# Optimization experiments

Hardware: AMD Instinct MI355X
Metric: run time of the kernel (lower is better)

Reference implementation:

```python
import jax, jax.numpy as jnp
import numpy as np

# ---- static config (mirrors Net.__init__) ----
N_NODES, N_EDGES = 4000, 20000
N_PROTS, D = 919, 512            # node_emb: Embedding(919, 512); F_in = D (divide_input=False)
TOWERS, F_OUT = 4, D // 4        # F_out = out_channels // towers = 128
EDGE_D = 50
N_GRAPHS, N_CLASSES = 32, 10
N_LAYERS = 2
EPS_BN, EPS_STD = 1e-5, 1e-5

# deg histogram passed to PNAConv; only avg_deg['log'] matters for the scalers used
DEG_HIST = np.array([0., 800., 1200., 900., 600., 300., 150., 50.])
AVG_DEG_LOG = float((np.log(np.arange(DEG_HIST.size) + 1.0) * DEG_HIST).sum() / DEG_HIST.sum())


def setup_inputs() -> dict:
    key = jax.random.key(0)
    ks = jax.random.split(key, 16)
    g = lambda i, shape, s=0.05: (jax.random.normal(ks[i], shape, jnp.float32) * s)
    return dict(
        node_emb_w=g(0, (N_PROTS, D), 0.1),
        edge_emb_w=g(1, (2, EDGE_D), 0.1),
        pe_w=g(2, (2, D)), pe_b=jnp.zeros((D,), jnp.float32),
        edge_enc_w=g(3, (N_LAYERS, EDGE_D, D)), edge_enc_b=jnp.zeros((N_LAYERS, D), jnp.float32),
        pre_w=g(4, (N_LAYERS, TOWERS, 3 * D, D)), pre_b=jnp.zeros((N_LAYERS, TOWERS, D), jnp.float32),
        post_w=g(5, (N_LAYERS, TOWERS, 13 * D, F_OUT)), post_b=jnp.zeros((N_LAYERS, TOWERS, F_OUT), jnp.float32),
        lin_w=g(6, (N_LAYERS, D, D)), lin_b=jnp.zeros((N_LAYERS, D), jnp.float32),
        bn_gamma=jnp.ones((N_LAYERS, D), jnp.float32), bn_beta=jnp.zeros((N_LAYERS, D), jnp.float32),
        acts=jax.random.normal(ks[7], (N_NODES, 2), jnp.float32),
        fc1_w=g(8, (D, 2 * D)), fc1_b=jnp.zeros((2 * D,), jnp.float32),
        fc_out_w=g(9, (2 * D, N_CLASSES)), fc_out_b=jnp.zeros((N_CLASSES,), jnp.float32),
        prelu_a=jnp.float32(0.25),
        global_idx=jax.random.randint(ks[10], (N_NODES,), 0, N_PROTS),
        sign=jax.random.randint(ks[11], (N_EDGES,), 0, 2),
        edge_index=jax.random.randint(ks[12], (2, N_EDGES), 0, N_NODES),
        batch=jnp.sort(jax.random.randint(ks[13], (N_NODES,), 0, N_GRAPHS)),
    )


def _pna_layer(x, src, dst, e, pre_w, pre_b, post_w, post_b, lin_w, lin_b):
    # x: [N, D], e: [E, D] (edge_encoder output), pre_w: [T, 3D, D], post_w: [T, 13D, F_OUT]
    N, E = x.shape[0], src.shape[0]
    # pre-NN on cat([x_i, x_j, edge_attr]) expressed as split matmuls (pre_layers=1 -> single Linear)
    Wi, Wj, We = pre_w[:, :D], pre_w[:, D:2 * D], pre_w[:, 2 * D:]
    m = (jnp.einsum('ef,tfd->etd', x[dst], Wi)
         + jnp.einsum('ef,tfd->etd', x[src], Wj)
         + jnp.einsum('ef,tfd->etd', e, We) + pre_b)          # [E, T, D]
    # multi-aggregation at destination nodes: mean / min / max / std
    cnt = jax.ops.segment_sum(jnp.ones((E,), m.dtype), dst, N)  # in-degree
    has = (cnt > 0)[:, None, None]
    deg = jnp.maximum(cnt, 1.0)[:, None, None]                  # clamp(1) as in PyG
    s1 = jax.ops.segment_sum(m, dst, N)
    s2 = jax.ops.segment_sum(m * m, dst, N)
    mean = s1 / deg
    std = jnp.sqrt(jax.nn.relu(s2 / deg - mean * mean) + EPS_STD)
    mn = jnp.where(has, jax.ops.segment_min(m, dst, N), 0.0)
    mx = jnp.where(has, jax.ops.segment_max(m, dst, N), 0.0)
    agg = jnp.concatenate([mean, mn, mx, std], axis=-1)         # [N, T, 4D]
    # degree scalers: identity, amplification, attenuation
    amp = jnp.log(deg + 1.0) / AVG_DEG_LOG
    out = jnp.concatenate([agg, agg * amp, agg / amp], axis=-1)  # [N, T, 12D]
    # post-NN on cat([x, out]) as split matmuls (post_layers=1)
    Wx, Wo = post_w[:, :D], post_w[:, D:]
    o = (jnp.einsum('nf,tfd->ntd', x, Wx)
         + jnp.einsum('ntf,tfd->ntd', out, Wo) + post_b)        # [N, T, F_OUT]
    return o.reshape(N, TOWERS * F_OUT) @ lin_w + lin_b         # [N, D]


def reference(node_emb_w, edge_emb_w, pe_w, pe_b, edge_enc_w, edge_enc_b,
              pre_w, pre_b, post_w, post_b, lin_w, lin_b, bn_gamma, bn_beta,
              acts, fc1_w, fc1_b, fc_out_w, fc_out_b, prelu_a,
              global_idx, sign, edge_index, batch):
    src, dst = edge_index[0], edge_index[1]
    x = node_emb_w[global_idx] + (acts @ pe_w + pe_b)           # node_emb + PostEncoding
    ea = edge_emb_w[sign]                                       # [E, 50]
    for l in range(N_LAYERS):
        e = ea @ edge_enc_w[l] + edge_enc_b[l]                  # shared edge encoder
        h = _pna_layer(x, src, dst, e, pre_w[l], pre_b[l], post_w[l], post_b[l], lin_w[l], lin_b[l])
        mu = h.mean(axis=0)
        var = ((h - mu) ** 2).mean(axis=0)                      # training-mode BatchNorm (biased var)
        x = jax.nn.relu(bn_gamma[l] * (h - mu) * jax.lax.rsqrt(var + EPS_BN) + bn_beta[l])
    pooled = jax.ops.segment_sum(x, batch, N_GRAPHS)            # global_add_pool
    z = pooled @ fc1_w + fc1_b
    z = jnp.where(z > 0, z, prelu_a * z)                        # PReLU
    logits = z @ fc_out_w + fc_out_b
    return jax.nn.log_softmax(logits, axis=-1)
```

## Files before the change

### kernel.cpp

```cpp
#include <hip/hip_runtime.h>
#include <hip/hip_bf16.h>
#include <float.h>

#define NN 4000
#define NE 20000
#define DD 512
#define NT 4
#define FO 128
#define NG 32
#define NC 10
#define XGW 4608
#define AVGLOG 1.2548916493836102f
#define EPS_STD_ 1e-5f
#define EPS_BN_ 1e-5f

typedef __bf16 bf16x8 __attribute__((ext_vector_type(8)));
typedef float  f32x4  __attribute__((ext_vector_type(4)));

__device__ __forceinline__ void async_copy16(const void* g, void* l) {
    __builtin_amdgcn_global_load_lds((const __attribute__((address_space(1))) void*)g,
                                     (__attribute__((address_space(3))) void*)l, 16, 0, 0);
}

template<int OUT_BF16, int HAS_BIAS>
__device__ __forceinline__ void mfma_core(
    const __bf16* __restrict__ A, int lda,
    const __bf16* __restrict__ BT, int ldbt,
    void* __restrict__ Cv, int ldc,
    const float* __restrict__ bias,
    int M, int K, int m0, int n0)
{
    __shared__ __bf16 As[128 * 32];
    __shared__ __bf16 Bs[128 * 32];
    const int tid = threadIdx.x;
    const int wave = tid >> 6, lane = tid & 63;
    const int wm = (wave >> 1) * 64, wn = (wave & 1) * 64;
    const int fr = lane & 15, fq = lane >> 4;
    const int fk = fq * 8;
    const int srow = lane >> 2;
    const int skc = (lane & 3) * 8;

    f32x4 acc[4][4];
    const f32x4 zero = {0.f, 0.f, 0.f, 0.f};
#pragma unroll
    for (int i = 0; i < 4; ++i)
#pragma unroll
        for (int j = 0; j < 4; ++j) acc[i][j] = zero;

    for (int k0 = 0; k0 < K; k0 += 32) {
#pragma unroll
        for (int q = 0; q < 2; ++q) {
            const int row = wave * 32 + q * 16 + srow;
            int ar = m0 + row; if (ar > M - 1) ar = M - 1;
            async_copy16(A + (size_t)ar * lda + k0 + skc, As + wave * 1024 + q * 512);
            async_copy16(BT + (size_t)(n0 + row) * ldbt + k0 + skc, Bs + wave * 1024 + q * 512);
        }
        __syncthreads();
        bf16x8 af[4], bfr[4];
#pragma unroll
        for (int mi = 0; mi < 4; ++mi) af[mi]  = *(const bf16x8*)(As + (wm + mi * 16 + fr) * 32 + fk);
#pragma unroll
        for (int ni = 0; ni < 4; ++ni) bfr[ni] = *(const bf16x8*)(Bs + (wn + ni * 16 + fr) * 32 + fk);
#pragma unroll
        for (int mi = 0; mi < 4; ++mi)
#pragma unroll
            for (int ni = 0; ni < 4; ++ni)
                acc[mi][ni] = __builtin_amdgcn_mfma_f32_16x16x32_bf16(af[mi], bfr[ni], acc[mi][ni], 0, 0, 0);
        __syncthreads();
    }
    float* Cf = (float*)Cv; __bf16* Cb = (__bf16*)Cv;
#pragma unroll
    for (int mi = 0; mi < 4; ++mi) {
#pragma unroll
        for (int ni = 0; ni < 4; ++ni) {
            const int col = n0 + wn + ni * 16 + fr;
            const int rb = m0 + wm + mi * 16 + fq * 4;
            const float bv = HAS_BIAS ? bias[col] : 0.f;
#pragma unroll
            for (int r = 0; r < 4; ++r) {
                const int rowc = rb + r;
                if (rowc < M) {
                    const float v = acc[mi][ni][r] + bv;
                    if (OUT_BF16) Cb[(size_t)rowc * ldc + col] = (__bf16)v;
                    else          Cf[(size_t)rowc * ldc + col] = v;
                }
            }
        }
    }
}

__global__ __launch_bounds__(256) void k_xg(const __bf16* __restrict__ XB, const __bf16* __restrict__ WCAT,
                                            __bf16* __restrict__ XG) {
    mfma_core<1, 0>(XB, 512, WCAT, 512, XG, XGW, nullptr, NN, 512,
                    blockIdx.y * 128, blockIdx.x * 128);
}

__global__ __launch_bounds__(256) void k_gw(const __bf16* __restrict__ AB, const __bf16* __restrict__ WTT,
                                            float* __restrict__ GWP) {
    const int t = blockIdx.z & 3, kh = blockIdx.z >> 2;
    const __bf16* A  = AB  + (size_t)t * 2048 + (size_t)kh * 1024;
    const __bf16* BT = WTT + (size_t)t * 384 * 2048 + (size_t)kh * 1024;
    float* C = GWP + (size_t)blockIdx.z * NN * 384;
    mfma_core<0, 0>(A, 8192, BT, 2048, C, 384, nullptr, NN, 1024,
                    blockIdx.y * 128, blockIdx.x * 128);
}

__global__ __launch_bounds__(256) void k_lin(const __bf16* __restrict__ OB, const __bf16* __restrict__ WLINT,
                                             const float* __restrict__ bl, float* __restrict__ H) {
    mfma_core<0, 1>(OB, 512, WLINT, 512, H, 512, bl, NN, 512,
                    blockIdx.y * 128, blockIdx.x * 128);
}

__device__ __forceinline__ void tr32(const float* __restrict__ S, int sld,
                                     __bf16* __restrict__ D, int dld) {
    __shared__ float t[32][33];
    const int x = threadIdx.x, y0 = threadIdx.y * 4;
#pragma unroll
    for (int i = 0; i < 4; ++i) t[y0 + i][x] = S[(size_t)(y0 + i) * sld + x];
    __syncthreads();
#pragma unroll
    for (int i = 0; i < 4; ++i) D[(size_t)(y0 + i) * dld + x] = (__bf16)t[x][y0 + i];
}

__global__ void k_tr(const float* __restrict__ pw, const float* __restrict__ pow_,
                     const float* __restrict__ lw,
                     __bf16* __restrict__ WCAT, __bf16* __restrict__ WTT, __bf16* __restrict__ WLINT) {
    int id = blockIdx.x;
    if (id < 2048) {
        const int z = id >> 8, r = id & 255;
        const int t = z & 3, half = z >> 2;
        const int x = r & 15, y = r >> 4;
        const float* S = pw + ((size_t)(t * 1536 + half * 512 + y * 32)) * 512 + x * 32;
        __bf16* D = WCAT + ((size_t)(half * 2048 + t * 512 + x * 32)) * 512 + y * 32;
        tr32(S, 512, D, 512);
    } else if (id < 2304) {
        const int id3 = id - 2048;
        const int t = id3 >> 6, r = id3 & 63;
        const int x = r & 3, y = r >> 2;
        const float* S = pow_ + ((size_t)(t * 6656 + y * 32)) * 128 + x * 32;
        __bf16* D = WCAT + ((size_t)(4096 + t * 128 + x * 32)) * 512 + y * 32;
        tr32(S, 128, D, 512);
    } else if (id < 5376) {
        const int id4 = id - 2304;
        const int z = id4 >> 8, r = id4 & 255;
        const int t = z / 3, w = z % 3;
        const int x = r & 3, y = r >> 2;
        const float* S = pow_ + ((size_t)(t * 6656 + 512 + w * 2048 + y * 32)) * 128 + x * 32;
        __bf16* D = WTT + (size_t)t * 384 * 2048 + ((size_t)(w * 128 + x * 32)) * 2048 + y * 32;
        tr32(S, 128, D, 2048);
    } else {
        const int r = id - 5376;
        const int x = r & 15, y = r >> 4;
        const float* S = lw + (size_t)y * 32 * 512 + x * 32;
        __bf16* D = WLINT + (size_t)x * 32 * 512 + y * 32;
        tr32(S, 512, D, 512);
    }
}

__global__ void k_count(const int* __restrict__ dst, int* __restrict__ cnt) {
    int e = blockIdx.x * 256 + threadIdx.x;
    if (e < NE) atomicAdd(&cnt[dst[e]], 1);
}

__global__ __launch_bounds__(1024) void k_scan(const int* __restrict__ cnt, int* __restrict__ offs,
                                               float* __restrict__ amp, float* __restrict__ ramp) {
    __shared__ int part[1024];
    const int t = threadIdx.x;
    const int base = t * 4;
    int loc[4]; int s = 0;
#pragma unroll
    for (int i = 0; i < 4; ++i) { int v = (base + i < NN) ? cnt[base + i] : 0; loc[i] = s; s += v; }
    part[t] = s;
    __syncthreads();
    for (int o = 1; o < 1024; o <<= 1) {
        int v = (t >= o) ? part[t - o] : 0;
        __syncthreads();
        part[t] += v;
        __syncthreads();
    }
    const int pre = (t > 0) ? part[t - 1] : 0;
#pragma unroll
    for (int i = 0; i < 4; ++i) if (base + i < NN) offs[base + i] = pre + loc[i];
    if (t == 1023) offs[NN] = part[1023];
    for (int n = t; n < NN; n += 1024) {
        float deg = fmaxf((float)cnt[n], 1.0f);
        float a = logf(deg + 1.0f) / AVGLOG;
        amp[n] = a; ramp[n] = 1.0f / a;
    }
}

__global__ void k_fill(const int* __restrict__ src, const int* __restrict__ dst,
                       const int* __restrict__ sgn, const int* __restrict__ offs,
                       int* __restrict__ fill, int* __restrict__ esrc, int* __restrict__ esgn) {
    int e = blockIdx.x * 256 + threadIdx.x;
    if (e < NE) {
        int d = dst[e];
        int pos = offs[d] + atomicAdd(&fill[d], 1);
        esrc[pos] = src[e];
        esgn[pos] = sgn[e];
    }
}

__global__ void k_build_x(const float* __restrict__ nemb, const float* __restrict__ acts,
                          const float* __restrict__ pew, const float* __restrict__ peb,
                          const int* __restrict__ gidx, float* __restrict__ X, __bf16* __restrict__ XB) {
    int idx = blockIdx.x * 256 + threadIdx.x;
    int n = idx >> 9, d = idx & 511;
    float v = nemb[(size_t)gidx[n] * DD + d] + acts[n * 2] * pew[d] + acts[n * 2 + 1] * pew[DD + d] + peb[d];
    X[idx] = v; XB[idx] = (__bf16)v;
}

__global__ __launch_bounds__(256) void k_ekem(const float* __restrict__ eemb, const float* __restrict__ eew,
                                              const float* __restrict__ eeb, const float* __restrict__ pw,
                                              const float* __restrict__ pb, float* __restrict__ EM) {
    __shared__ float EKs[1024];
    const int tid = threadIdx.x;
    for (int i = tid; i < 1024; i += 256) {
        int k = i >> 9, d = i & 511;
        float s = eeb[d];
        for (int f = 0; f < 50; ++f) s += eemb[k * 50 + f] * eew[(size_t)f * 512 + d];
        EKs[i] = s;
    }
    __syncthreads();
    const int idx = blockIdx.x * 256 + tid;
    const int k = idx >> 11, g = idx & 2047;
    const int t = g >> 9, d = g & 511;
    const float* ek = EKs + k * 512;
    const float* W = pw + ((size_t)t * 1536 + 1024) * 512 + d;
    float s = pb[g];
    for (int f = 0; f < 512; ++f) s += ek[f] * W[(size_t)f * 512];
    EM[idx] = s;
}

__global__ __launch_bounds__(256) void k_agg(const __bf16* __restrict__ XG, const float* __restrict__ EM,
                                             const int* __restrict__ offs, const int* __restrict__ cnt,
                                             const int* __restrict__ esrc, const int* __restrict__ esgn,
                                             __bf16* __restrict__ AB) {
    const int n = blockIdx.x;
    const int g = threadIdx.x * 8;
    float xid[8], em0[8], em1[8];
    {
        bf16x8 xb = *(const bf16x8*)(XG + (size_t)n * XGW + g);
#pragma unroll
        for (int i = 0; i < 8; ++i) xid[i] = (float)xb[i];
    }
    *(float4*)&em0[0] = *(const float4*)&EM[g];
    *(float4*)&em0[4] = *(const float4*)&EM[g + 4];
    *(float4*)&em1[0] = *(const float4*)&EM[2048 + g];
    *(float4*)&em1[4] = *(const float4*)&EM[2048 + g + 4];
    float s1[8], s2[8], mn[8], mx[8];
#pragma unroll
    for (int i = 0; i < 8; ++i) { s1[i] = 0.f; s2[i] = 0.f; mn[i] = FLT_MAX; mx[i] = -FLT_MAX; }
    const int j0 = offs[n], j1 = offs[n + 1];
    for (int j = j0; j < j1; ++j) {
        const int s = esrc[j];
        const int sg = esgn[j];
        bf16x8 xv = *(const bf16x8*)(XG + (size_t)s * XGW + 2048 + g);
#pragma unroll
        for (int i = 0; i < 8; ++i) {
            float m = xid[i] + (float)xv[i] + (sg ? em1[i] : em0[i]);
            s1[i] += m; s2[i] += m * m;
            mn[i] = fminf(mn[i], m); mx[i] = fmaxf(mx[i], m);
        }
    }
    const int c = cnt[n];
    const float deg = fmaxf((float)c, 1.0f);
    const float rdeg = 1.0f / deg;
    bf16x8 vmean, vmn, vmx, vsd;
#pragma unroll
    for (int i = 0; i < 8; ++i) {
        float mean = s1[i] * rdeg;
        float var = s2[i] * rdeg - mean * mean;
        float sd = sqrtf(fmaxf(var, 0.f) + EPS_STD_);
        float mnv = (c == 0) ? 0.f : mn[i];
        float mxv = (c == 0) ? 0.f : mx[i];
        vmean[i] = (__bf16)mean; vmn[i] = (__bf16)mnv; vmx[i] = (__bf16)mxv; vsd[i] = (__bf16)sd;
    }
    const int t = g >> 9, d = g & 511;
    __bf16* base = AB + (size_t)n * 8192 + (size_t)t * 2048 + d;
    *(bf16x8*)(base + 0 * DD) = vmean;
    *(bf16x8*)(base + 1 * DD) = vmn;
    *(bf16x8*)(base + 2 * DD) = vmx;
    *(bf16x8*)(base + 3 * DD) = vsd;
}

__global__ void k_combine(const __bf16* __restrict__ XG, const float* __restrict__ GWP,
                          const float* __restrict__ amp, const float* __restrict__ ramp,
                          const float* __restrict__ pb, __bf16* __restrict__ OB) {
    int idx = blockIdx.x * 256 + threadIdx.x;
    int n = idx >> 9, c = idx & 511;
    int t = c >> 7, o = c & 127;
    const float* ga = GWP + ((size_t)t) * NN * 384 + (size_t)n * 384;
    const float* gb = GWP + ((size_t)(4 + t)) * NN * 384 + (size_t)n * 384;
    float w1 = ga[o] + gb[o];
    float w2 = ga[128 + o] + gb[128 + o];
    float w3 = ga[256 + o] + gb[256 + o];
    float gx = (float)XG[(size_t)n * XGW + 4096 + c];
    float v = gx + w1 + amp[n] * w2 + ramp[n] * w3 + pb[c];
    OB[idx] = (__bf16)v;
}

__global__ void k_bnstat(const float* __restrict__ H, float* __restrict__ BN) {
    int cidx = blockIdx.x * 256 + threadIdx.x;
    int r0 = blockIdx.y * 125;
    float s = 0.f, q = 0.f;
    for (int r = r0; r < r0 + 125; ++r) { float v = H[(size_t)r * DD + cidx]; s += v; q += v * v; }
    atomicAdd(&BN[cidx], s); atomicAdd(&BN[DD + cidx], q);
}

__global__ void k_bnapply(const float* __restrict__ H, const float* __restrict__ BN,
                          const float* __restrict__ gamma, const float* __restrict__ beta,
                          float* __restrict__ X, __bf16* __restrict__ XB) {
    int idx = blockIdx.x * 256 + threadIdx.x;
    int d = idx & 511;
    float mu = BN[d] * (1.0f / NN);
    float var = BN[DD + d] * (1.0f / NN) - mu * mu;
    float v = gamma[d] * (H[idx] - mu) * rsqrtf(var + EPS_BN_) + beta[d];
    v = fmaxf(v, 0.f);
    X[idx] = v; XB[idx] = (__bf16)v;
}

__global__ void k_pool(const float* __restrict__ X, const int* __restrict__ batch, float* __restrict__ PL) {
    int idx = blockIdx.x * 256 + threadIdx.x;
    int n = idx >> 9, d = idx & 511;
    atomicAdd(&PL[(size_t)batch[n] * DD + d], X[idx]);
}

__global__ void k_fc1(const float* __restrict__ PL, const float* __restrict__ W1,
                      const float* __restrict__ b1, const float* __restrict__ pa, float* __restrict__ Z) {
    int idx = blockIdx.x * 256 + threadIdx.x;
    int g = idx >> 10, j = idx & 1023;
    float s = b1[j];
    const float* p = PL + (size_t)g * DD;
    for (int f = 0; f < DD; ++f) s += p[f] * W1[(size_t)f * 1024 + j];
    float a = *pa;
    Z[idx] = s > 0.f ? s : a * s;
}

__global__ __launch_bounds__(64) void k_out(const float* __restrict__ Z, const float* __restrict__ Wo,
                                            const float* __restrict__ bo, float* __restrict__ out) {
    int g = blockIdx.x, t = threadIdx.x;
    float part[NC];
#pragma unroll
    for (int c = 0; c < NC; ++c) part[c] = 0.f;
    for (int f = t; f < 1024; f += 64) {
        float zv = Z[g * 1024 + f];
#pragma unroll
        for (int c = 0; c < NC; ++c) part[c] += zv * Wo[(size_t)f * NC + c];
    }
#pragma unroll
    for (int off = 32; off > 0; off >>= 1)
#pragma unroll
        for (int c = 0; c < NC; ++c) part[c] += __shfl_down(part[c], off);
    if (t == 0) {
        float lg[NC], mxv = -FLT_MAX;
#pragma unroll
        for (int c = 0; c < NC; ++c) { lg[c] = part[c] + bo[c]; mxv = fmaxf(mxv, lg[c]); }
        float se = 0.f;
#pragma unroll
        for (int c = 0; c < NC; ++c) se += expf(lg[c] - mxv);
        float lse = mxv + logf(se);
#pragma unroll
        for (int c = 0; c < NC; ++c) out[g * NC + c] = lg[c] - lse;
    }
}

extern "C" void kernel_launch(void* const* d_in, const int* in_sizes, int n_in,
                              void* d_out, int out_size, void* d_ws, size_t ws_size,
                              hipStream_t stream) {
    const float* node_emb_w = (const float*)d_in[0];
    const float* edge_emb_w = (const float*)d_in[1];
    const float* pe_w   = (const float*)d_in[2];
    const float* pe_b   = (const float*)d_in[3];
    const float* edge_enc_w = (const float*)d_in[4];
    const float* edge_enc_b = (const float*)d_in[5];
    const float* pre_w  = (const float*)d_in[6];
    const float* pre_b  = (const float*)d_in[7];
    const float* post_w = (const float*)d_in[8];
    const float* post_b = (const float*)d_in[9];
    const float* lin_w  = (const float*)d_in[10];
    const float* lin_b  = (const float*)d_in[11];
    const float* bn_gamma = (const float*)d_in[12];
    const float* bn_beta  = (const float*)d_in[13];
    const float* acts   = (const float*)d_in[14];
    const float* fc1_w  = (const float*)d_in[15];
    const float* fc1_b  = (const float*)d_in[16];
    const float* fc_out_w = (const float*)d_in[17];
    const float* fc_out_b = (const float*)d_in[18];
    const float* prelu_a  = (const float*)d_in[19];
    const int* global_idx = (const int*)d_in[20];
    const int* sgn        = (const int*)d_in[21];
    const int* edge_index = (const int*)d_in[22];
    const int* batch      = (const int*)d_in[23];
    float* out = (float*)d_out;

    char* W = (char*)d_ws;
    size_t off = 0;
    auto alloc = [&](size_t bytes) { void* p = W + off; off += (bytes + 63) & ~(size_t)63; return p; };
    float*  X     = (float*)alloc((size_t)NN * DD * 4);
    __bf16* XB    = (__bf16*)alloc((size_t)NN * DD * 2);
    float*  H     = (float*)alloc((size_t)NN * DD * 4);
    __bf16* XG    = (__bf16*)alloc((size_t)NN * XGW * 2);
    __bf16* AB    = (__bf16*)alloc((size_t)NN * 8192 * 2);
    float*  GWP   = (float*)alloc((size_t)8 * NN * 384 * 4);
    __bf16* OB    = (__bf16*)alloc((size_t)NN * DD * 2);
    __bf16* WCAT  = (__bf16*)alloc((size_t)XGW * 512 * 2);
    __bf16* WTT   = (__bf16*)alloc((size_t)NT * 384 * 2048 * 2);
    __bf16* WLINT = (__bf16*)alloc((size_t)512 * 512 * 2);
    float*  EM    = (float*)alloc(2 * 2048 * 4);
    float*  BN    = (float*)alloc(2 * 512 * 4);
    float*  PL    = (float*)alloc((size_t)NG * DD * 4);
    float*  ZB    = (float*)alloc((size_t)NG * 1024 * 4);
    float*  AMP   = (float*)alloc(NN * 4);
    float*  RAMP  = (float*)alloc(NN * 4);
    int*    CNT   = (int*)alloc(NN * 4);
    int*    OFFS  = (int*)alloc((NN + 1) * 4);
    int*    FILL  = (int*)alloc(NN * 4);
    int*    ESRC  = (int*)alloc(NE * 4);
    int*    ESGN  = (int*)alloc(NE * 4);

    const int* src = edge_index;
    const int* dst = edge_index + NE;

    hipMemsetAsync(CNT, 0, NN * sizeof(int), stream);
    hipMemsetAsync(FILL, 0, NN * sizeof(int), stream);
    k_count<<<(NE + 255) / 256, 256, 0, stream>>>(dst, CNT);
    k_scan<<<1, 1024, 0, stream>>>(CNT, OFFS, AMP, RAMP);
    k_fill<<<(NE + 255) / 256, 256, 0, stream>>>(src, dst, sgn, OFFS, FILL, ESRC, ESGN);
    k_build_x<<<NN * DD / 256, 256, 0, stream>>>(node_emb_w, acts, pe_w, pe_b, global_idx, X, XB);

    for (int l = 0; l < 2; ++l) {
        const float* pre_w_l  = pre_w  + (size_t)l * NT * 3 * DD * DD;
        const float* pre_b_l  = pre_b  + (size_t)l * NT * DD;
        const float* post_w_l = post_w + (size_t)l * NT * 6656 * FO;
        const float* post_b_l = post_b + (size_t)l * NT * FO;
        const float* lin_w_l  = lin_w  + (size_t)l * DD * DD;
        const float* lin_b_l  = lin_b  + (size_t)l * DD;
        const float* eew_l    = edge_enc_w + (size_t)l * 50 * DD;
        const float* eeb_l    = edge_enc_b + (size_t)l * DD;

        k_tr<<<5632, dim3(32, 8), 0, stream>>>(pre_w_l, post_w_l, lin_w_l, WCAT, WTT, WLINT);
        k_ekem<<<16, 256, 0, stream>>>(edge_emb_w, eew_l, eeb_l, pre_w_l, pre_b_l, EM);

        k_xg<<<dim3(36, 32), 256, 0, stream>>>(XB, WCAT, XG);
        k_agg<<<NN, 256, 0, stream>>>(XG, EM, OFFS, CNT, ESRC, ESGN, AB);
        k_gw<<<dim3(3, 32, 8), 256, 0, stream>>>(AB, WTT, GWP);
        k_combine<<<NN * DD / 256, 256, 0, stream>>>(XG, GWP, AMP, RAMP, post_b_l, OB);
        k_lin<<<dim3(4, 32), 256, 0, stream>>>(OB, WLINT, lin_b_l, H);

        hipMemsetAsync(BN, 0, 2 * DD * sizeof(float), stream);
        k_bnstat<<<dim3(2, 32), 256, 0, stream>>>(H, BN);
        k_bnapply<<<NN * DD / 256, 256, 0, stream>>>(H, BN, bn_gamma + (size_t)l * DD, bn_beta + (size_t)l * DD, X, XB);
    }

    hipMemsetAsync(PL, 0, NG * DD * sizeof(float), stream);
    k_pool<<<NN * DD / 256, 256, 0, stream>>>(X, batch, PL);
    k_fc1<<<NG * 1024 / 256, 256, 0, stream>>>(PL, fc1_w, fc1_b, prelu_a, ZB);
    k_out<<<NG, 64, 0, stream>>>(ZB, fc_out_w, fc_out_b, out);
}
```

Before: 570.5 us.

## Fuse combine, BN stats, pooling and head into GEMM epilogues and merge launches

The tower GEMM k_gw is rewritten as a full-K 32x384 tile that applies the scaler combine in its epilogue, which removes the split-K fp32 partial buffer and the separate combine kernel. k_lin now accumulates batch-norm sums in its epilogue, k_bnapply pools directly on the last layer, and fc1, the output layer and log_softmax are merged into one head kernel. The build_x work is merged into the scan launch, the fp32 X buffer is dropped, and the edge-matrix kernel is parallelised across 64 blocks. The cost is fewer blocks in k_gw (500, each running a long K loop), which may reduce occupancy and latency hiding.

Result: slower. 582.2 us (+2.0%).

```diff
diff --git a/kernel.cpp b/kernel.cpp
--- a/kernel.cpp
+++ b/kernel.cpp
@@ -22,12 +22,10 @@
                                      (__attribute__((address_space(3))) void*)l, 16, 0, 0);
 }
 
-template<int OUT_BF16, int HAS_BIAS>
-__device__ __forceinline__ void mfma_core(
+__device__ __forceinline__ void mfma_core128(
     const __bf16* __restrict__ A, int lda,
     const __bf16* __restrict__ BT, int ldbt,
-    void* __restrict__ Cv, int ldc,
-    const float* __restrict__ bias,
+    __bf16* __restrict__ C, int ldc,
     int M, int K, int m0, int n0)
 {
     __shared__ __bf16 As[128 * 32];
@@ -68,47 +66,176 @@
                 acc[mi][ni] = __builtin_amdgcn_mfma_f32_16x16x32_bf16(af[mi], bfr[ni], acc[mi][ni], 0, 0, 0);
         __syncthreads();
     }
-    float* Cf = (float*)Cv; __bf16* Cb = (__bf16*)Cv;
 #pragma unroll
     for (int mi = 0; mi < 4; ++mi) {
 #pragma unroll
         for (int ni = 0; ni < 4; ++ni) {
             const int col = n0 + wn + ni * 16 + fr;
             const int rb = m0 + wm + mi * 16 + fq * 4;
-            const float bv = HAS_BIAS ? bias[col] : 0.f;
 #pragma unroll
             for (int r = 0; r < 4; ++r) {
                 const int rowc = rb + r;
-                if (rowc < M) {
+                if (rowc < M) C[(size_t)rowc * ldc + col] = (__bf16)acc[mi][ni][r];
+            }
+        }
+    }
+}
+
+__global__ __launch_bounds__(256) void k_xg(const __bf16* __restrict__ XB, const __bf16* __restrict__ WCAT,
+                                            __bf16* __restrict__ XG) {
+    mfma_core128(XB, 512, WCAT, 512, XG, XGW, NN, 512, blockIdx.y * 128, blockIdx.x * 128);
+}
+
+__global__ __launch_bounds__(256) void k_gw(const __bf16* __restrict__ AB, const __bf16* __restrict__ WTT,
+                                            const __bf16* __restrict__ XG,
+                                            const float* __restrict__ amp, const float* __restrict__ ramp,
+                                            const float* __restrict__ pb, __bf16* __restrict__ OB,
+                                            float* __restrict__ BN, float* __restrict__ PL, int zero_pl) {
+    const int t = blockIdx.y;
+    const int n0 = blockIdx.x * 32;
+    __shared__ __bf16 As[32 * 32];
+    __shared__ __bf16 Bs[384 * 32];
+    __shared__ float  Ep[32][388];
+    const int tid = threadIdx.x;
+    const int wave = tid >> 6, lane = tid & 63;
+    const int fr = lane & 15, fq = lane >> 4;
+    const int wn = wave * 96;
+
+    f32x4 acc[2][6];
+    const f32x4 zero = {0.f, 0.f, 0.f, 0.f};
+#pragma unroll
+    for (int i = 0; i < 2; ++i)
+#pragma unroll
+        for (int j = 0; j < 6; ++j) acc[i][j] = zero;
+
+    const __bf16* Abase = AB + (size_t)n0 * 8192 + (size_t)t * 2048;
+    const __bf16* Bbase = WTT + (size_t)t * 384 * 2048;
+    const int ar = tid >> 2, akc = (tid & 3) * 8;
+
+    for (int k0 = 0; k0 < 2048; k0 += 32) {
+        if (wave < 2)
+            async_copy16(Abase + (size_t)ar * 8192 + k0 + akc, As + tid * 8);
+#pragma unroll
+        for (int i = 0; i < 6; ++i) {
+            const int cb = tid + 256 * i;
+            const int br = cb >> 2, bkc = (cb & 3) * 8;
+            async_copy16(Bbase + (size_t)br * 2048 + k0 + bkc, Bs + cb * 8);
+        }
+        __syncthreads();
+        bf16x8 a[2], b[6];
+#pragma unroll
+        for (int mi = 0; mi < 2; ++mi) a[mi] = *(const bf16x8*)(As + (mi * 16 + fr) * 32 + fq * 8);
+#pragma unroll
+        for (int ni = 0; ni < 6; ++ni) b[ni] = *(const bf16x8*)(Bs + (wn + ni * 16 + fr) * 32 + fq * 8);
+#pragma unroll
+        for (int mi = 0; mi < 2; ++mi)
+#pragma unroll
+            for (int ni = 0; ni < 6; ++ni)
+                acc[mi][ni] = __builtin_amdgcn_mfma_f32_16x16x32_bf16(a[mi], b[ni], acc[mi][ni], 0, 0, 0);
+        __syncthreads();
+    }
+#pragma unroll
+    for (int mi = 0; mi < 2; ++mi)
+#pragma unroll
+        for (int ni = 0; ni < 6; ++ni)
+#pragma unroll
+            for (int r = 0; r < 4; ++r)
+                Ep[mi * 16 + fq * 4 + r][wn + ni * 16 + fr] = acc[mi][ni][r];
+    __syncthreads();
+    const int row = tid >> 3, o0 = (tid & 7) * 16;
+    const int n = n0 + row;
+    const float av = amp[n], rv = ramp[n];
+    bf16x8 gx0 = *(const bf16x8*)(XG + (size_t)n * XGW + 4096 + t * 128 + o0);
+    bf16x8 gx1 = *(const bf16x8*)(XG + (size_t)n * XGW + 4096 + t * 128 + o0 + 8);
+    bf16x8 ov0, ov1;
+#pragma unroll
+    for (int u = 0; u < 8; ++u) {
+        int o = o0 + u;
+        float v = (float)gx0[u] + Ep[row][o] + av * Ep[row][128 + o] + rv * Ep[row][256 + o] + pb[t * 128 + o];
+        ov0[u] = (__bf16)v;
+    }
+#pragma unroll
+    for (int u = 0; u < 8; ++u) {
+        int o = o0 + 8 + u;
+        float v = (float)gx1[u] + Ep[row][o] + av * Ep[row][128 + o] + rv * Ep[row][256 + o] + pb[t * 128 + o];
+        ov1[u] = (__bf16)v;
+    }
+    *(bf16x8*)(OB + (size_t)n * 512 + t * 128 + o0) = ov0;
+    *(bf16x8*)(OB + (size_t)n * 512 + t * 128 + o0 + 8) = ov1;
+    if (blockIdx.x == 0 && blockIdx.y == 0) {
+        BN[tid] = 0.f; BN[256 + tid] = 0.f; BN[512 + tid] = 0.f; BN[768 + tid] = 0.f;
+        if (zero_pl)
+            for (int i = tid; i < NG * DD; i += 256) PL[i] = 0.f;
+    }
+}
+
+__global__ __launch_bounds__(256) void k_lin(const __bf16* __restrict__ OB, const __bf16* __restrict__ WLINT,
+                                             const float* __restrict__ bl, float* __restrict__ H,
+                                             float* __restrict__ BN) {
+    const int n0c = blockIdx.x * 128, m0 = blockIdx.y * 64;
+    __shared__ __bf16 As[64 * 32];
+    __shared__ __bf16 Bs[128 * 32];
+    __shared__ float bnS[128], bnQ[128];
+    const int tid = threadIdx.x;
+    if (tid < 128) { bnS[tid] = 0.f; bnQ[tid] = 0.f; }
+    const int wave = tid >> 6, lane = tid & 63;
+    const int wr = wave >> 1, wc = wave & 1;
+    const int fr = lane & 15, fq = lane >> 4;
+    f32x4 acc[2][4];
+    const f32x4 zero = {0.f, 0.f, 0.f, 0.f};
+#pragma unroll
+    for (int i = 0; i < 2; ++i)
+#pragma unroll
+        for (int j = 0; j < 4; ++j) acc[i][j] = zero;
+
+    const int ar = tid >> 2, akc = (tid & 3) * 8;
+    int arow = m0 + ar; if (arow > NN - 1) arow = NN - 1;
+    for (int k0 = 0; k0 < 512; k0 += 32) {
+        async_copy16(OB + (size_t)arow * 512 + k0 + akc, As + tid * 8);
+#pragma unroll
+        for (int i = 0; i < 2; ++i) {
+            const int cb = tid + 256 * i;
+            const int br = cb >> 2, bkc = (cb & 3) * 8;
+            async_copy16(WLINT + (size_t)(n0c + br) * 512 + k0 + bkc, Bs + cb * 8);
+        }
+        __syncthreads();
+        bf16x8 a[2], b[4];
+#pragma unroll
+        for (int mi = 0; mi < 2; ++mi) a[mi] = *(const bf16x8*)(As + (wr * 32 + mi * 16 + fr) * 32 + fq * 8);
+#pragma unroll
+        for (int ni = 0; ni < 4; ++ni) b[ni] = *(const bf16x8*)(Bs + (wc * 64 + ni * 16 + fr) * 32 + fq * 8);
+#pragma unroll
+        for (int mi = 0; mi < 2; ++mi)
+#pragma unroll
+            for (int ni = 0; ni < 4; ++ni)
+                acc[mi][ni] = __builtin_amdgcn_mfma_f32_16x16x32_bf16(a[mi], b[ni], acc[mi][ni], 0, 0, 0);
+        __syncthreads();
+    }
+#pragma unroll
+    for (int ni = 0; ni < 4; ++ni) {
+        const int lc = wc * 64 + ni * 16 + fr;
+        const int col = n0c + lc;
+        const float bv = bl[col];
+        float s = 0.f, q = 0.f;
+#pragma unroll
+        for (int mi = 0; mi < 2; ++mi) {
+#pragma unroll
+            for (int r = 0; r < 4; ++r) {
+                const int rowc = m0 + wr * 32 + mi * 16 + fq * 4 + r;
+                if (rowc < NN) {
                     const float v = acc[mi][ni][r] + bv;
-                    if (OUT_BF16) Cb[(size_t)rowc * ldc + col] = (__bf16)v;
-                    else          Cf[(size_t)rowc * ldc + col] = v;
+                    H[(size_t)rowc * 512 + col] = v;
+                    s += v; q += v * v;
                 }
             }
         }
-    }
-}
-
-__global__ __launch_bounds__(256) void k_xg(const __bf16* __restrict__ XB, const __bf16* __restrict__ WCAT,
-                                            __bf16* __restrict__ XG) {
-    mfma_core<1, 0>(XB, 512, WCAT, 512, XG, XGW, nullptr, NN, 512,
-                    blockIdx.y * 128, blockIdx.x * 128);
-}
-
-__global__ __launch_bounds__(256) void k_gw(const __bf16* __restrict__ AB, const __bf16* __restrict__ WTT,
-                                            float* __restrict__ GWP) {
-    const int t = blockIdx.z & 3, kh = blockIdx.z >> 2;
-    const __bf16* A  = AB  + (size_t)t * 2048 + (size_t)kh * 1024;
-    const __bf16* BT = WTT + (size_t)t * 384 * 2048 + (size_t)kh * 1024;
-    float* C = GWP + (size_t)blockIdx.z * NN * 384;
-    mfma_core<0, 0>(A, 8192, BT, 2048, C, 384, nullptr, NN, 1024,
-                    blockIdx.y * 128, blockIdx.x * 128);
-}
-
-__global__ __launch_bounds__(256) void k_lin(const __bf16* __restrict__ OB, const __bf16* __restrict__ WLINT,
-                                             const float* __restrict__ bl, float* __restrict__ H) {
-    mfma_core<0, 1>(OB, 512, WLINT, 512, H, 512, bl, NN, 512,
-                    blockIdx.y * 128, blockIdx.x * 128);
+        atomicAdd(&bnS[lc], s); atomicAdd(&bnQ[lc], q);
+    }
+    __syncthreads();
+    if (tid < 128) {
+        atomicAdd(&BN[n0c + tid], bnS[tid]);
+        atomicAdd(&BN[512 + n0c + tid], bnQ[tid]);
+    }
 }
 
 __device__ __forceinline__ void tr32(const float* __restrict__ S, int sld,
@@ -162,30 +289,40 @@
     if (e < NE) atomicAdd(&cnt[dst[e]], 1);
 }
 
-__global__ __launch_bounds__(1024) void k_scan(const int* __restrict__ cnt, int* __restrict__ offs,
-                                               float* __restrict__ amp, float* __restrict__ ramp) {
-    __shared__ int part[1024];
+__global__ __launch_bounds__(1024) void k_scan_bx(const int* __restrict__ cnt, int* __restrict__ offs,
+                                                  float* __restrict__ amp, float* __restrict__ ramp,
+                                                  const float* __restrict__ nemb, const float* __restrict__ acts,
+                                                  const float* __restrict__ pew, const float* __restrict__ peb,
+                                                  const int* __restrict__ gidx, __bf16* __restrict__ XB) {
     const int t = threadIdx.x;
-    const int base = t * 4;
-    int loc[4]; int s = 0;
-#pragma unroll
-    for (int i = 0; i < 4; ++i) { int v = (base + i < NN) ? cnt[base + i] : 0; loc[i] = s; s += v; }
-    part[t] = s;
-    __syncthreads();
-    for (int o = 1; o < 1024; o <<= 1) {
-        int v = (t >= o) ? part[t - o] : 0;
-        __syncthreads();
-        part[t] += v;
-        __syncthreads();
-    }
-    const int pre = (t > 0) ? part[t - 1] : 0;
-#pragma unroll
-    for (int i = 0; i < 4; ++i) if (base + i < NN) offs[base + i] = pre + loc[i];
-    if (t == 1023) offs[NN] = part[1023];
-    for (int n = t; n < NN; n += 1024) {
-        float deg = fmaxf((float)cnt[n], 1.0f);
-        float a = logf(deg + 1.0f) / AVGLOG;
-        amp[n] = a; ramp[n] = 1.0f / a;
+    if (blockIdx.x == 0) {
+        __shared__ int part[1024];
+        const int base = t * 4;
+        int loc[4]; int s = 0;
+#pragma unroll
+        for (int i = 0; i < 4; ++i) { int v = (base + i < NN) ? cnt[base + i] : 0; loc[i] = s; s += v; }
+        part[t] = s;
+        __syncthreads();
+        for (int o = 1; o < 1024; o <<= 1) {
+            int v = (t >= o) ? part[t - o] : 0;
+            __syncthreads();
+            part[t] += v;
+            __syncthreads();
+        }
+        const int pre = (t > 0) ? part[t - 1] : 0;
+#pragma unroll
+        for (int i = 0; i < 4; ++i) if (base + i < NN) offs[base + i] = pre + loc[i];
+        if (t == 1023) offs[NN] = part[1023];
+        for (int n = t; n < NN; n += 1024) {
+            float deg = fmaxf((float)cnt[n], 1.0f);
+            float a = logf(deg + 1.0f) / AVGLOG;
+            amp[n] = a; ramp[n] = 1.0f / a;
+        }
+    } else {
+        const int idx = (blockIdx.x - 1) * 1024 + t;
+        const int n = idx >> 9, d = idx & 511;
+        float v = nemb[(size_t)gidx[n] * DD + d] + acts[n * 2] * pew[d] + acts[n * 2 + 1] * pew[DD + d] + peb[d];
+        XB[idx] = (__bf16)v;
     }
 }
 
@@ -201,35 +338,36 @@
     }
 }
 
-__global__ void k_build_x(const float* __restrict__ nemb, const float* __restrict__ acts,
-                          const float* __restrict__ pew, const float* __restrict__ peb,
-                          const int* __restrict__ gidx, float* __restrict__ X, __bf16* __restrict__ XB) {
-    int idx = blockIdx.x * 256 + threadIdx.x;
-    int n = idx >> 9, d = idx & 511;
-    float v = nemb[(size_t)gidx[n] * DD + d] + acts[n * 2] * pew[d] + acts[n * 2 + 1] * pew[DD + d] + peb[d];
-    X[idx] = v; XB[idx] = (__bf16)v;
-}
-
-__global__ __launch_bounds__(256) void k_ekem(const float* __restrict__ eemb, const float* __restrict__ eew,
-                                              const float* __restrict__ eeb, const float* __restrict__ pw,
-                                              const float* __restrict__ pb, float* __restrict__ EM) {
-    __shared__ float EKs[1024];
+__global__ __launch_bounds__(256) void k_em(const float* __restrict__ eemb, const float* __restrict__ eew,
+                                            const float* __restrict__ eeb, const float* __restrict__ pw,
+                                            const float* __restrict__ pb, float* __restrict__ EM) {
+    __shared__ float eks[512];
+    __shared__ float part[4][64];
     const int tid = threadIdx.x;
-    for (int i = tid; i < 1024; i += 256) {
-        int k = i >> 9, d = i & 511;
-        float s = eeb[d];
-        for (int f = 0; f < 50; ++f) s += eemb[k * 50 + f] * eew[(size_t)f * 512 + d];
-        EKs[i] = s;
-    }
-    __syncthreads();
-    const int idx = blockIdx.x * 256 + tid;
-    const int k = idx >> 11, g = idx & 2047;
+    const int k = blockIdx.x >> 5;
+    const int g0 = (blockIdx.x & 31) * 64;
+#pragma unroll
+    for (int h = 0; h < 2; ++h) {
+        const int f = tid + h * 256;
+        float s = eeb[f];
+        for (int c = 0; c < 50; ++c) s += eemb[k * 50 + c] * eew[(size_t)c * 512 + f];
+        eks[f] = s;
+    }
+    __syncthreads();
+    const int wave = tid >> 6, lane = tid & 63;
+    const int g = g0 + lane;
     const int t = g >> 9, d = g & 511;
-    const float* ek = EKs + k * 512;
-    const float* W = pw + ((size_t)t * 1536 + 1024) * 512 + d;
-    float s = pb[g];
-    for (int f = 0; f < 512; ++f) s += ek[f] * W[(size_t)f * 512];
-    EM[idx] = s;
+    const float* Wp = pw + ((size_t)(t * 1536 + 1024)) * 512 + d;
+    float s = 0.f;
+    const int f0 = wave * 128;
+#pragma unroll 4
+    for (int f = f0; f < f0 + 128; ++f) s += eks[f] * Wp[(size_t)f * 512];
+    part[wave][lane] = s;
+    __syncthreads();
+    if (tid < 64) {
+        const int gg = g0 + tid;
+        EM[k * 2048 + gg] = pb[gg] + part[0][tid] + part[1][tid] + part[2][tid] + part[3][tid];
+    }
 }
 
 __global__ __launch_bounds__(256) void k_agg(const __bf16* __restrict__ XG, const float* __restrict__ EM,
@@ -284,84 +422,73 @@
     *(bf16x8*)(base + 3 * DD) = vsd;
 }
 
-__global__ void k_combine(const __bf16* __restrict__ XG, const float* __restrict__ GWP,
-                          const float* __restrict__ amp, const float* __restrict__ ramp,
-                          const float* __restrict__ pb, __bf16* __restrict__ OB) {
-    int idx = blockIdx.x * 256 + threadIdx.x;
-    int n = idx >> 9, c = idx & 511;
-    int t = c >> 7, o = c & 127;
-    const float* ga = GWP + ((size_t)t) * NN * 384 + (size_t)n * 384;
-    const float* gb = GWP + ((size_t)(4 + t)) * NN * 384 + (size_t)n * 384;
-    float w1 = ga[o] + gb[o];
-    float w2 = ga[128 + o] + gb[128 + o];
-    float w3 = ga[256 + o] + gb[256 + o];
-    float gx = (float)XG[(size_t)n * XGW + 4096 + c];
-    float v = gx + w1 + amp[n] * w2 + ramp[n] * w3 + pb[c];
-    OB[idx] = (__bf16)v;
-}
-
-__global__ void k_bnstat(const float* __restrict__ H, float* __restrict__ BN) {
-    int cidx = blockIdx.x * 256 + threadIdx.x;
-    int r0 = blockIdx.y * 125;
-    float s = 0.f, q = 0.f;
-    for (int r = r0; r < r0 + 125; ++r) { float v = H[(size_t)r * DD + cidx]; s += v; q += v * v; }
-    atomicAdd(&BN[cidx], s); atomicAdd(&BN[DD + cidx], q);
-}
-
 __global__ void k_bnapply(const float* __restrict__ H, const float* __restrict__ BN,
                           const float* __restrict__ gamma, const float* __restrict__ beta,
-                          float* __restrict__ X, __bf16* __restrict__ XB) {
+                          __bf16* __restrict__ XB, float* __restrict__ PL,
+                          const int* __restrict__ batch, int last) {
     int idx = blockIdx.x * 256 + threadIdx.x;
-    int d = idx & 511;
+    int n = idx >> 9, d = idx & 511;
     float mu = BN[d] * (1.0f / NN);
-    float var = BN[DD + d] * (1.0f / NN) - mu * mu;
+    float var = BN[512 + d] * (1.0f / NN) - mu * mu;
     float v = gamma[d] * (H[idx] - mu) * rsqrtf(var + EPS_BN_) + beta[d];
     v = fmaxf(v, 0.f);
-    X[idx] = v; XB[idx] = (__bf16)v;
-}
-
-__global__ void k_pool(const float* __restrict__ X, const int* __restrict__ batch, float* __restrict__ PL) {
-    int idx = blockIdx.x * 256 + threadIdx.x;
-    int n = idx >> 9, d = idx & 511;
-    atomicAdd(&PL[(size_t)batch[n] * DD + d], X[idx]);
-}
-
-__global__ void k_fc1(const float* __restrict__ PL, const float* __restrict__ W1,
-                      const float* __restrict__ b1, const float* __restrict__ pa, float* __restrict__ Z) {
-    int idx = blockIdx.x * 256 + threadIdx.x;
-    int g = idx >> 10, j = idx & 1023;
-    float s = b1[j];
-    const float* p = PL + (size_t)g * DD;
-    for (int f = 0; f < DD; ++f) s += p[f] * W1[(size_t)f * 1024 + j];
-    float a = *pa;
-    Z[idx] = s > 0.f ? s : a * s;
-}
-
-__global__ __launch_bounds__(64) void k_out(const float* __restrict__ Z, const float* __restrict__ Wo,
-                                            const float* __restrict__ bo, float* __restrict__ out) {
-    int g = blockIdx.x, t = threadIdx.x;
-    float part[NC];
-#pragma unroll
-    for (int c = 0; c < NC; ++c) part[c] = 0.f;
-    for (int f = t; f < 1024; f += 64) {
-        float zv = Z[g * 1024 + f];
-#pragma unroll
-        for (int c = 0; c < NC; ++c) part[c] += zv * Wo[(size_t)f * NC + c];
+    if (last) atomicAdd(&PL[(size_t)batch[n] * DD + d], v);
+    else XB[idx] = (__bf16)v;
+}
+
+__global__ __launch_bounds__(256) void k_head(const float* __restrict__ PL, const float* __restrict__ W1,
+                                              const float* __restrict__ b1, const float* __restrict__ Wo,
+                                              const float* __restrict__ bo, const float* __restrict__ pa,
+                                              float* __restrict__ out) {
+    __shared__ float pl[512];
+    __shared__ float zz[1024];
+    __shared__ float lgs[NC];
+    const int g = blockIdx.x, tid = threadIdx.x;
+    pl[tid] = PL[(size_t)g * 512 + tid];
+    pl[tid + 256] = PL[(size_t)g * 512 + 256 + tid];
+    if (tid < NC) lgs[tid] = bo[tid];
+    __syncthreads();
+    const float a = *pa;
+#pragma unroll
+    for (int h = 0; h < 4; ++h) {
+        const int j = tid + h * 256;
+        float s0 = 0.f, s1 = 0.f, s2 = 0.f, s3 = 0.f;
+        for (int f = 0; f < 512; f += 4) {
+            s0 += pl[f + 0] * W1[(size_t)(f + 0) * 1024 + j];
+            s1 += pl[f + 1] * W1[(size_t)(f + 1) * 1024 + j];
+            s2 += pl[f + 2] * W1[(size_t)(f + 2) * 1024 + j];
+            s3 += pl[f + 3] * W1[(size_t)(f + 3) * 1024 + j];
+        }
+        float s = b1[j] + ((s0 + s1) + (s2 + s3));
+        zz[j] = s > 0.f ? s : a * s;
+    }
+    __syncthreads();
+    float p[NC];
+#pragma unroll
+    for (int c = 0; c < NC; ++c) p[c] = 0.f;
+    for (int f = tid; f < 1024; f += 256) {
+        const float z = zz[f];
+#pragma unroll
+        for (int c = 0; c < NC; ++c) p[c] += z * Wo[(size_t)f * NC + c];
     }
 #pragma unroll
     for (int off = 32; off > 0; off >>= 1)
 #pragma unroll
-        for (int c = 0; c < NC; ++c) part[c] += __shfl_down(part[c], off);
-    if (t == 0) {
-        float lg[NC], mxv = -FLT_MAX;
-#pragma unroll
-        for (int c = 0; c < NC; ++c) { lg[c] = part[c] + bo[c]; mxv = fmaxf(mxv, lg[c]); }
+        for (int c = 0; c < NC; ++c) p[c] += __shfl_down(p[c], off);
+    if ((tid & 63) == 0)
+#pragma unroll
+        for (int c = 0; c < NC; ++c) atomicAdd(&lgs[c], p[c]);
+    __syncthreads();
+    if (tid == 0) {
+        float mxv = -FLT_MAX;
+#pragma unroll
+        for (int c = 0; c < NC; ++c) mxv = fmaxf(mxv, lgs[c]);
         float se = 0.f;
 #pragma unroll
-        for (int c = 0; c < NC; ++c) se += expf(lg[c] - mxv);
-        float lse = mxv + logf(se);
-#pragma unroll
-        for (int c = 0; c < NC; ++c) out[g * NC + c] = lg[c] - lse;
+        for (int c = 0; c < NC; ++c) se += expf(lgs[c] - mxv);
+        const float lse = mxv + logf(se);
+#pragma unroll
+        for (int c = 0; c < NC; ++c) out[g * NC + c] = lgs[c] - lse;
     }
 }
 
@@ -397,37 +524,33 @@
     char* W = (char*)d_ws;
     size_t off = 0;
     auto alloc = [&](size_t bytes) { void* p = W + off; off += (bytes + 63) & ~(size_t)63; return p; };
-    float*  X     = (float*)alloc((size_t)NN * DD * 4);
     __bf16* XB    = (__bf16*)alloc((size_t)NN * DD * 2);
     float*  H     = (float*)alloc((size_t)NN * DD * 4);
     __bf16* XG    = (__bf16*)alloc((size_t)NN * XGW * 2);
     __bf16* AB    = (__bf16*)alloc((size_t)NN * 8192 * 2);
-    float*  GWP   = (float*)alloc((size_t)8 * NN * 384 * 4);
     __bf16* OB    = (__bf16*)alloc((size_t)NN * DD * 2);
     __bf16* WCAT  = (__bf16*)alloc((size_t)XGW * 512 * 2);
     __bf16* WTT   = (__bf16*)alloc((size_t)NT * 384 * 2048 * 2);
     __bf16* WLINT = (__bf16*)alloc((size_t)512 * 512 * 2);
     float*  EM    = (float*)alloc(2 * 2048 * 4);
-    float*  BN    = (float*)alloc(2 * 512 * 4);
+    float*  BN    = (float*)alloc(1024 * 4);
     float*  PL    = (float*)alloc((size_t)NG * DD * 4);
-    float*  ZB    = (float*)alloc((size_t)NG * 1024 * 4);
     float*  AMP   = (float*)alloc(NN * 4);
     float*  RAMP  = (float*)alloc(NN * 4);
     int*    CNT   = (int*)alloc(NN * 4);
+    int*    FILL  = (int*)alloc(NN * 4);
     int*    OFFS  = (int*)alloc((NN + 1) * 4);
-    int*    FILL  = (int*)alloc(NN * 4);
     int*    ESRC  = (int*)alloc(NE * 4);
     int*    ESGN  = (int*)alloc(NE * 4);
 
     const int* src = edge_index;
     const int* dst = edge_index + NE;
 
-    hipMemsetAsync(CNT, 0, NN * sizeof(int), stream);
-    hipMemsetAsync(FILL, 0, NN * sizeof(int), stream);
+    hipMemsetAsync(CNT, 0, 2 * NN * sizeof(int), stream);
     k_count<<<(NE + 255) / 256, 256, 0, stream>>>(dst, CNT);
-    k_scan<<<1, 1024, 0, stream>>>(CNT, OFFS, AMP, RAMP);
+    k_scan_bx<<<2001, 1024, 0, stream>>>(CNT, OFFS, AMP, RAMP,
+                                         node_emb_w, acts, pe_w, pe_b, global_idx, XB);
     k_fill<<<(NE + 255) / 256, 256, 0, stream>>>(src, dst, sgn, OFFS, FILL, ESRC, ESGN);
-    k_build_x<<<NN * DD / 256, 256, 0, stream>>>(node_emb_w, acts, pe_w, pe_b, global_idx, X, XB);
 
     for (int l = 0; l < 2; ++l) {
         const float* pre_w_l  = pre_w  + (size_t)l * NT * 3 * DD * DD;
@@ -440,21 +563,14 @@
         const float* eeb_l    = edge_enc_b + (size_t)l * DD;
 
         k_tr<<<5632, dim3(32, 8), 0, stream>>>(pre_w_l, post_w_l, lin_w_l, WCAT, WTT, WLINT);
-        k_ekem<<<16, 256, 0, stream>>>(edge_emb_w, eew_l, eeb_l, pre_w_l, pre_b_l, EM);
-
+        k_em<<<64, 256, 0, stream>>>(edge_emb_w, eew_l, eeb_l, pre_w_l, pre_b_l, EM);
         k_xg<<<dim3(36, 32), 256, 0, stream>>>(XB, WCAT, XG);
         k_agg<<<NN, 256, 0, stream>>>(XG, EM, OFFS, CNT, ESRC, ESGN, AB);
-        k_gw<<<dim3(3, 32, 8), 256, 0, stream>>>(AB, WTT, GWP);
-        k_combine<<<NN * DD / 256, 256, 0, stream>>>(XG, GWP, AMP, RAMP, post_b_l, OB);
-        k_lin<<<dim3(4, 32), 256, 0, stream>>>(OB, WLINT, lin_b_l, H);
-
-        hipMemsetAsync(BN, 0, 2 * DD * sizeof(float), stream);
-        k_bnstat<<<dim3(2, 32), 256, 0, stream>>>(H, BN);
-        k_bnapply<<<NN * DD / 256, 256, 0, stream>>>(H, BN, bn_gamma + (size_t)l * DD, bn_beta + (size_t)l * DD, X, XB);
-    }
-
-    hipMemsetAsync(PL, 0, NG * DD * sizeof(float), stream);
-    k_pool<<<NN * DD / 256, 256, 0, stream>>>(X, batch, PL);
-    k_fc1<<<NG * 1024 / 256, 256, 0, stream>>>(PL, fc1_w, fc1_b, prelu_a, ZB);
-    k_out<<<NG, 64, 0, stream>>>(ZB, fc_out_w, fc_out_b, out);
-}
+        k_gw<<<dim3(125, 4), 256, 0, stream>>>(AB, WTT, XG, AMP, RAMP, post_b_l, OB, BN, PL, l == 1);
+        k_lin<<<dim3(4, 63), 256, 0, stream>>>(OB, WLINT, lin_b_l, H, BN);
+        k_bnapply<<<NN * DD / 256, 256, 0, stream>>>(H, BN, bn_gamma + (size_t)l * DD,
+                                                     bn_beta + (size_t)l * DD, XB, PL, batch, l == 1);
+    }
+
+    k_head<<<NG, 256, 0, stream>>>(PL, fc1_w, fc1_b, fc_out_w, fc_out_b, prelu_a, out);
+}
```
